# Optimization experiments

Measured on AMD Instinct MI355X. Metric: run time of the kernel, lower is better.

## Reference

```python
import jax, jax.numpy as jnp
import numpy as np

H = W = 512
A = 256  # number of projection angles


def setup_inputs() -> dict:
    key = jax.random.key(0)
    k1, k2 = jax.random.split(key)
    data = jax.random.normal(k1, (1, 1, H, W), dtype=jnp.float32)
    # angles uniform in [0, pi) -- realistic tomographic scan range
    angles = jax.random.uniform(k2, (A,), dtype=jnp.float32) * np.float32(np.pi)
    return {"data": data, "angles": angles}


def _radon(data, angles):
    B, C, h, w = data.shape  # B == C == 1 structurally required by the torch module
    nA = angles.shape[0]
    cos = jnp.cos(angles)
    sin = jnp.sin(angles)

    # F.affine_grid(align_corners=False) base coordinates: pixel centers in [-1, 1]
    xs = (2.0 * jnp.arange(w, dtype=data.dtype) + 1.0) / w - 1.0  # [W]
    ys = (2.0 * jnp.arange(h, dtype=data.dtype) + 1.0) / h - 1.0  # [H]
    by, bx = jnp.meshgrid(ys, xs, indexing="ij")  # [H,W]

    # theta built from -angles: rows [cos a, sin a, 0; -sin a, cos a, 0]
    gx = cos[:, None, None] * bx + sin[:, None, None] * by  # [A,H,W]
    gy = -sin[:, None, None] * bx + cos[:, None, None] * by  # [A,H,W]

    # grid_sample(align_corners=False): unnormalize to input pixel coords
    ix = ((gx + 1.0) * w - 1.0) * 0.5
    iy = ((gy + 1.0) * h - 1.0) * 0.5

    x0 = jnp.floor(ix).astype(jnp.int32)
    y0 = jnp.floor(iy).astype(jnp.int32)
    x1 = x0 + 1
    y1 = y0 + 1
    wx1 = ix - x0.astype(data.dtype)
    wx0 = 1.0 - wx1
    wy1 = iy - y0.astype(data.dtype)
    wy0 = 1.0 - wy1

    img = data[0, 0]  # [H,W]

    def gather(yy, xx):
        # zero padding: out-of-range taps contribute 0
        valid = (xx >= 0) & (xx < w) & (yy >= 0) & (yy < h)
        v = img[jnp.clip(yy, 0, h - 1), jnp.clip(xx, 0, w - 1)]
        return jnp.where(valid, v, jnp.zeros((), data.dtype))

    rotated = (wy0 * (wx0 * gather(y0, x0) + wx1 * gather(y0, x1))
               + wy1 * (wx0 * gather(y1, x0) + wx1 * gather(y1, x1)))  # [A,H,W]

    proj = jnp.sum(rotated, axis=1)  # sum over height -> [A,W]
    return proj.reshape(1, 1, nA, w)


def reference(data, angles):
    return _radon(data, angles)
```

## Files before the change

### kernel.cpp

```cpp
#include <hip/hip_runtime.h>


#define HH 512
#define WW 512
#define NA 256
#define XC 64
#define YC 64
#define NXC 8
#define NYC 8
#define NW 8
#define RM 96
#define SM 97
#define PAD 112
#define PW (WW + 2 * PAD)
#define PH (HH + 2 * PAD)

typedef float f32x2 __attribute__((ext_vector_type(2)));

__global__ __launch_bounds__(256) void pad_kernel(
    const float* __restrict__ img, float* __restrict__ P)
{
    const int c = blockIdx.x * 256 + threadIdx.x;
    const int r = blockIdx.y;
    if (c >= PW) return;
    const int gr = r - PAD, gc = c - PAD;
    float v = 0.0f;
    if ((unsigned)gr < (unsigned)HH && (unsigned)gc < (unsigned)WW)
        v = img[gr * WW + gc];
    P[r * PW + c] = v;
}

template <int S, bool PADDED>
__device__ __forceinline__ float radon_chunks(
    const float* __restrict__ src, float* __restrict__ tile,
    const float s, const float c, const int lane, const int wid, const int x0)
{
    const float u  = (float)(x0 + lane) + (0.5f - 256.0f);
    const float u0 = (float)x0 + (0.5f - 256.0f);
    const float u1 = u0 + 63.0f;

    const float cu0 = c * u0, cu1 = c * u1;
    const float cumin = fminf(cu0, cu1), cumax = fmaxf(cu0, cu1);
    const float su0 = -s * u0, su1 = -s * u1;
    const float sumin = fminf(su0, su1), sumax = fmaxf(su0, su1);

    const float bcc = fmaf(c, u, 255.5f);
    const float brc = fmaf(-s, u, 255.5f);

    const float* __restrict__ Porg =
        PADDED ? (src + PAD * PW + PAD) : src;

    f32x2 accT = {0.0f, 0.0f}, accB = {0.0f, 0.0f};

    for (int yc = 0; yc < NYC; ++yc) {
        const float v0 = (float)(yc * YC) + (0.5f - 256.0f);
        const float v1 = v0 + 63.0f;

        const float sv0 = s * v0, sv1 = s * v1;
        const float cv0 = c * v0, cv1 = c * v1;
        const float cvmin = fminf(cv0, cv1), cvmax = fmaxf(cv0, cv1);

        const float cx_min = cumin + sv0 + 255.5f;
        const float cx_max = cumax + sv1 + 255.5f;
        const float rx_min = sumin + cvmin + 255.5f;
        const float rx_max = sumax + cvmax + 255.5f;

        const int c_lo = (int)floorf(cx_min);
        const int c_hi = (int)floorf(cx_max) + 1;
        const int r_lo = (int)floorf(rx_min);
        const int r_hi = (int)floorf(rx_max) + 1;

        if (c_lo > WW - 1 || c_hi < 0 || r_lo > HH - 1 || r_hi < 0) continue;

        __syncthreads();

        if (PADDED) {
            if (lane < 23) {
                const float* g = Porg + (r_lo + wid) * PW + c_lo + lane * 4;
                int loff = wid * S;
#pragma unroll
                for (int k = 0; k < 12; ++k) {
                    __builtin_amdgcn_global_load_lds(
                        (const __attribute__((address_space(1))) void*)g,
                        (__attribute__((address_space(3))) void*)&tile[loff],
                        16, 0, 0);
                    g += NW * PW;
                    loff += NW * S;
                }
            }
        } else {
            for (int r = wid; r < RM; r += NW) {
                const int gr = r_lo + r;
                const bool row_ok = ((unsigned)gr < (unsigned)HH);
                const float* __restrict__ rowp = src + gr * WW;
                for (int cc = lane; cc < 92; cc += 64) {
                    const int gc = c_lo + cc;
                    float v = 0.0f;
                    if (row_ok && (unsigned)gc < (unsigned)WW)
                        v = rowp[gc];
                    tile[r * S + cc] = v;
                }
            }
        }

        __syncthreads();

        const float bc = bcc - (float)c_lo;
        const float br = brc - (float)r_lo;
        const float vyb = v0 + (float)(wid * 8);
        const float cx0 = fmaf(s, vyb, bc);
        const float rx0 = fmaf(c, vyb, br);

#pragma unroll
        for (int i = 0; i < 8; ++i) {
            const float cxl = fmaf(s, (float)i, cx0);
            const float rxl = fmaf(c, (float)i, rx0);
            const int ci = (int)cxl;
            const int ri = (int)rxl;
            const float wx1 = __builtin_amdgcn_fractf(cxl);
            const float wy1 = __builtin_amdgcn_fractf(rxl);
            const float wy0 = 1.0f - wy1;

            __builtin_assume(ri >= 0 && ri < RM - 1);
            __builtin_assume(ci >= 0 && ci < 92);
            const int ad = ri * S + ci;

            f32x2 vt, vb;
            vt.x = tile[ad];     vt.y = tile[ad + 1];
            vb.x = tile[ad + S]; vb.y = tile[ad + S + 1];

            const f32x2 wx = {1.0f - wx1, wx1};
            accT = __builtin_elementwise_fma(wx * wy0, vt, accT);
            accB = __builtin_elementwise_fma(wx * wy1, vb, accB);
        }
    }

    return (accT.x + accT.y) + (accB.x + accB.y);
}

template <bool PADDED>
__global__ __launch_bounds__(512, 8) void radon_kernel(
    const float* __restrict__ src,
    const float* __restrict__ angles, float* __restrict__ out)
{
    __shared__ float tile[RM * SM];

    const int tid  = threadIdx.x;
    const int lane = tid & 63;
    const int wid  = tid >> 6;

    const int a  = blockIdx.x >> 3;
    const int x0 = (blockIdx.x & 7) * XC;

    float s, c;
    sincosf(angles[a], &s, &c);

    float acc;
    if (c >= 0.0f)
        acc = radon_chunks<95, PADDED>(src, tile, s, c, lane, wid, x0);
    else
        acc = radon_chunks<97, PADDED>(src, tile, s, c, lane, wid, x0);

    __syncthreads();
    tile[tid] = acc;
    __syncthreads();
    if (tid < 64) {
        float r = tile[tid];
#pragma unroll
        for (int k = 1; k < NW; ++k) r += tile[k * 64 + tid];
        out[a * WW + x0 + tid] = r;
    }
}

extern "C" void kernel_launch(void* const* d_in, const int* in_sizes, int n_in,
                              void* d_out, int out_size, void* d_ws, size_t ws_size,
                              hipStream_t stream) {
    const float* img    = (const float*)d_in[0];
    const float* angles = (const float*)d_in[1];
    float* out = (float*)d_out;
    float* P   = (float*)d_ws;

    const bool padded = (ws_size >= (size_t)PW * PH * sizeof(float));

    if (padded) {
        pad_kernel<<<dim3((PW + 255) / 256, PH), 256, 0, stream>>>(img, P);
        radon_kernel<true><<<dim3(NA * NXC), 512, 0, stream>>>(P, angles, out);
    } else {
        radon_kernel<false><<<dim3(NA * NXC), 512, 0, stream>>>(img, angles, out);
    }
}
```

Before: 111.4 us.

## Pack vertically adjacent pixels as fp16 pairs and use dot2 for bilinear taps

The padding kernel now stores each pixel together with the pixel below it as a packed fp16 pair in one 32-bit word. The inner loop then needs two LDS loads instead of four, and does the vertical interpolation with fdot2 instructions. This cuts LDS traffic and FMA count per sample, but drops the image values and vertical weights to fp16, which loses precision. The reduction buffer is split into its own shared array, which adds LDS usage.

```diff
diff --git a/kernel.cpp b/kernel.cpp
--- a/kernel.cpp
+++ b/kernel.cpp
@@ -15,24 +15,39 @@
 #define PW (WW + 2 * PAD)
 #define PH (HH + 2 * PAD)
 
-typedef float f32x2 __attribute__((ext_vector_type(2)));
-
-__global__ __launch_bounds__(256) void pad_kernel(
-    const float* __restrict__ img, float* __restrict__ P)
+typedef __fp16 h2 __attribute__((ext_vector_type(2)));
+
+#if __has_builtin(__builtin_amdgcn_fdot2)
+#define FDOT2(a, b, cc) __builtin_amdgcn_fdot2((a), (b), (cc), false)
+#else
+static __device__ __forceinline__ float FDOT2(h2 a, h2 b, float cc) {
+    return fmaf((float)a.x, (float)b.x, fmaf((float)a.y, (float)b.y, cc));
+}
+#endif
+
+static __device__ __forceinline__ unsigned pack_pair(float v0, float v1) {
+    h2 p = __builtin_amdgcn_cvt_pkrtz(v0, v1);
+    return __builtin_bit_cast(unsigned, p);
+}
+
+__global__ __launch_bounds__(256) void padpack_kernel(
+    const float* __restrict__ img, unsigned* __restrict__ Pv)
 {
     const int c = blockIdx.x * 256 + threadIdx.x;
     const int r = blockIdx.y;
     if (c >= PW) return;
     const int gr = r - PAD, gc = c - PAD;
-    float v = 0.0f;
-    if ((unsigned)gr < (unsigned)HH && (unsigned)gc < (unsigned)WW)
-        v = img[gr * WW + gc];
-    P[r * PW + c] = v;
+    float v0 = 0.0f, v1 = 0.0f;
+    if ((unsigned)gc < (unsigned)WW) {
+        if ((unsigned)gr       < (unsigned)HH) v0 = img[gr * WW + gc];
+        if ((unsigned)(gr + 1) < (unsigned)HH) v1 = img[(gr + 1) * WW + gc];
+    }
+    Pv[r * PW + c] = pack_pair(v0, v1);
 }
 
 template <int S, bool PADDED>
 __device__ __forceinline__ float radon_chunks(
-    const float* __restrict__ src, float* __restrict__ tile,
+    const void* __restrict__ srcv, unsigned* __restrict__ tile,
     const float s, const float c, const int lane, const int wid, const int x0)
 {
     const float u  = (float)(x0 + lane) + (0.5f - 256.0f);
@@ -47,10 +62,10 @@
     const float bcc = fmaf(c, u, 255.5f);
     const float brc = fmaf(-s, u, 255.5f);
 
-    const float* __restrict__ Porg =
-        PADDED ? (src + PAD * PW + PAD) : src;
-
-    f32x2 accT = {0.0f, 0.0f}, accB = {0.0f, 0.0f};
+    const unsigned* __restrict__ Porg =
+        (const unsigned*)srcv + (PADDED ? (PAD * PW + PAD) : 0);
+
+    float acc = 0.0f;
 
     for (int yc = 0; yc < NYC; ++yc) {
         const float v0 = (float)(yc * YC) + (0.5f - 256.0f);
@@ -76,7 +91,7 @@
 
         if (PADDED) {
             if (lane < 23) {
-                const float* g = Porg + (r_lo + wid) * PW + c_lo + lane * 4;
+                const unsigned* g = Porg + (r_lo + wid) * PW + c_lo + lane * 4;
                 int loff = wid * S;
 #pragma unroll
                 for (int k = 0; k < 12; ++k) {
@@ -89,16 +104,17 @@
                 }
             }
         } else {
+            const float* __restrict__ img = (const float*)srcv;
             for (int r = wid; r < RM; r += NW) {
                 const int gr = r_lo + r;
-                const bool row_ok = ((unsigned)gr < (unsigned)HH);
-                const float* __restrict__ rowp = src + gr * WW;
                 for (int cc = lane; cc < 92; cc += 64) {
                     const int gc = c_lo + cc;
-                    float v = 0.0f;
-                    if (row_ok && (unsigned)gc < (unsigned)WW)
-                        v = rowp[gc];
-                    tile[r * S + cc] = v;
+                    float a0 = 0.0f, a1 = 0.0f;
+                    if ((unsigned)gc < (unsigned)WW) {
+                        if ((unsigned)gr       < (unsigned)HH) a0 = img[gr * WW + gc];
+                        if ((unsigned)(gr + 1) < (unsigned)HH) a1 = img[(gr + 1) * WW + gc];
+                    }
+                    tile[r * S + cc] = pack_pair(a0, a1);
                 }
             }
         }
@@ -119,31 +135,34 @@
             const int ri = (int)rxl;
             const float wx1 = __builtin_amdgcn_fractf(cxl);
             const float wy1 = __builtin_amdgcn_fractf(rxl);
+            const float wx0 = 1.0f - wx1;
             const float wy0 = 1.0f - wy1;
+            const h2 wy = __builtin_amdgcn_cvt_pkrtz(wy0, wy1);
 
             __builtin_assume(ri >= 0 && ri < RM - 1);
             __builtin_assume(ci >= 0 && ci < 92);
             const int ad = ri * S + ci;
 
-            f32x2 vt, vb;
-            vt.x = tile[ad];     vt.y = tile[ad + 1];
-            vb.x = tile[ad + S]; vb.y = tile[ad + S + 1];
-
-            const f32x2 wx = {1.0f - wx1, wx1};
-            accT = __builtin_elementwise_fma(wx * wy0, vt, accT);
-            accB = __builtin_elementwise_fma(wx * wy1, vb, accB);
+            const unsigned w0 = tile[ad];
+            const unsigned w1 = tile[ad + 1];
+
+            const float left  = FDOT2(__builtin_bit_cast(h2, w0), wy, 0.0f);
+            const float right = FDOT2(__builtin_bit_cast(h2, w1), wy, 0.0f);
+            acc = fmaf(wx0, left, acc);
+            acc = fmaf(wx1, right, acc);
         }
     }
 
-    return (accT.x + accT.y) + (accB.x + accB.y);
+    return acc;
 }
 
 template <bool PADDED>
 __global__ __launch_bounds__(512, 8) void radon_kernel(
-    const float* __restrict__ src,
+    const void* __restrict__ src,
     const float* __restrict__ angles, float* __restrict__ out)
 {
-    __shared__ float tile[RM * SM];
+    __shared__ unsigned tile[RM * SM];
+    __shared__ float red[512];
 
     const int tid  = threadIdx.x;
     const int lane = tid & 63;
@@ -162,12 +181,12 @@
         acc = radon_chunks<97, PADDED>(src, tile, s, c, lane, wid, x0);
 
     __syncthreads();
-    tile[tid] = acc;
+    red[tid] = acc;
     __syncthreads();
     if (tid < 64) {
-        float r = tile[tid];
+        float r = red[tid];
 #pragma unroll
-        for (int k = 1; k < NW; ++k) r += tile[k * 64 + tid];
+        for (int k = 1; k < NW; ++k) r += red[k * 64 + tid];
         out[a * WW + x0 + tid] = r;
     }
 }
@@ -177,15 +196,15 @@
                               hipStream_t stream) {
     const float* img    = (const float*)d_in[0];
     const float* angles = (const float*)d_in[1];
-    float* out = (float*)d_out;
-    float* P   = (float*)d_ws;
-
-    const bool padded = (ws_size >= (size_t)PW * PH * sizeof(float));
+    float* out   = (float*)d_out;
+    unsigned* Pv = (unsigned*)d_ws;
+
+    const bool padded = (ws_size >= (size_t)PW * PH * sizeof(unsigned));
 
     if (padded) {
-        pad_kernel<<<dim3((PW + 255) / 256, PH), 256, 0, stream>>>(img, P);
-        radon_kernel<true><<<dim3(NA * NXC), 512, 0, stream>>>(P, angles, out);
+        padpack_kernel<<<dim3((PW + 255) / 256, PH), 256, 0, stream>>>(img, Pv);
+        radon_kernel<true><<<dim3(NA * NXC), 512, 0, stream>>>((const void*)Pv, angles, out);
     } else {
-        radon_kernel<false><<<dim3(NA * NXC), 512, 0, stream>>>(img, angles, out);
-    }
-}
+        radon_kernel<false><<<dim3(NA * NXC), 512, 0, stream>>>((const void*)img, angles, out);
+    }
+}
```

New measurement: 114.3 us. 2.6% more time.
